# Kernel tuning notes

Measured on AMD Instinct MI355X. Metric: run time of the kernel, lower is better.

The kernel has to match this reference:

```python
import jax, jax.numpy as jnp
import numpy as np

# SamplesLoss('sinkhorn', p=2, blur=0.05, scaling=0.5, diameter=2.0, debias=True, backend='tensorized')
P = 2
BLUR = 0.05
SCALING = 0.5
DIAMETER = 2.0


def epsilon_schedule(p, diameter, blur, scaling):
    # geomloss epsilon annealing: diameter^p -> blur^p, geometric in eps
    eps_list = (
        [diameter ** p]
        + [np.exp(e) for e in np.arange(p * np.log(diameter), p * np.log(blur), p * np.log(scaling))]
        + [blur ** p]
    )
    return [float(e) for e in eps_list]


def softmin(eps, C, h):
    # soft C-transform: f_i = -eps * log sum_j exp(h_j - C_ij/eps)
    # C: (B,N,M), h: (B,M) -> (B,N)
    return -eps * jax.scipy.special.logsumexp(h[:, None, :] - C / eps, axis=2)


def sq_cost(x, y):
    # SqDist(x,y)/2 : (B,N,D),(B,M,D) -> (B,N,M)
    x2 = jnp.sum(x * x, axis=-1)[:, :, None]
    y2 = jnp.sum(y * y, axis=-1)[:, None, :]
    return (x2 + y2 - 2.0 * jnp.einsum('bnd,bmd->bnm', x, y)) * 0.5


def setup_inputs() -> dict:
    key = jax.random.key(0)
    k1, k2 = jax.random.split(key)
    x = jax.random.uniform(k1, (8, 2048, 3), dtype=jnp.float32)
    y = jax.random.uniform(k2, (8, 2048, 3), dtype=jnp.float32)
    return {"x": x, "y": y}


def reference(x, y):
    B, N, _ = x.shape
    M = y.shape[1]
    # uniform weights (SamplesLoss default when only point clouds are given)
    a_log = jnp.full((B, N), -float(np.log(N)), dtype=x.dtype)
    b_log = jnp.full((B, M), -float(np.log(M)), dtype=y.dtype)

    C_xy = sq_cost(x, y)                 # (B,N,M)
    C_yx = jnp.swapaxes(C_xy, 1, 2)      # (B,M,N)
    C_xx = sq_cost(x, x)                 # (B,N,N) debias term
    C_yy = sq_cost(y, y)                 # (B,M,M) debias term

    eps_list = epsilon_schedule(P, DIAMETER, BLUR, SCALING)

    # initialization at the coarsest temperature (balanced OT: damping = 1)
    eps0 = eps_list[0]
    f_aa = softmin(eps0, C_xx, a_log)
    g_bb = softmin(eps0, C_yy, b_log)
    g_ab = softmin(eps0, C_yx, a_log)
    f_ba = softmin(eps0, C_xy, b_log)

    # symmetric Sinkhorn loop with epsilon scaling (no grad tracked in torch here)
    for eps in eps_list:
        ft_ba = softmin(eps, C_xy, b_log + g_ab / eps)
        gt_ab = softmin(eps, C_yx, a_log + f_ba / eps)
        f_ba = 0.5 * (f_ba + ft_ba)
        g_ab = 0.5 * (g_ab + gt_ab)
        ft_aa = softmin(eps, C_xx, a_log + f_aa / eps)
        gt_bb = softmin(eps, C_yy, b_log + g_bb / eps)
        f_aa = 0.5 * (f_aa + ft_aa)
        g_bb = 0.5 * (g_bb + gt_bb)

    # last extrapolation step, with detached dual potentials (torch .detach())
    eps = eps_list[-1]
    sg = jax.lax.stop_gradient
    f_ba, g_ab = (
        softmin(eps, C_xy, b_log + sg(g_ab) / eps),
        softmin(eps, C_yx, a_log + sg(f_ba) / eps),
    )
    f_aa = softmin(eps, C_xx, a_log + sg(f_aa) / eps)
    g_bb = softmin(eps, C_yy, b_log + sg(g_bb) / eps)

    # debiased Sinkhorn divergence, batch mode -> (B,)
    a = jnp.exp(a_log)
    b = jnp.exp(b_log)
    return jnp.sum(a * (f_ba - f_aa), axis=-1) + jnp.sum(b * (g_ab - g_bb), axis=-1)
```

## Files before the change

kernel.cpp:

```cpp
#include <hip/hip_runtime.h>
#include <math.h>

#define BATCH 8
#define NPTS 2048
#define THREADS 256
#define HALF_COLS 1024
#define TILES_H 32
#define ROWS_PER_BLOCK 64
#define LOG_M 7.62559580411076

typedef __attribute__((ext_vector_type(8)))  __bf16 bf16x8;
typedef __attribute__((ext_vector_type(16))) float  f32x16;

union FragU { unsigned short u[8]; uint4 v; };

__device__ __forceinline__ unsigned short f2bf(float f) {
    union { float f; unsigned u; } x; x.f = f;
    unsigned r = x.u + 0x7FFFu + ((x.u >> 16) & 1u);
    return (unsigned short)(r >> 16);
}
__device__ __forceinline__ float bf2f(unsigned short b) {
    union { unsigned u; float f; } x; x.u = ((unsigned)b) << 16;
    return x.f;
}

__global__ __launch_bounds__(THREADS) void softmin_pass(
    const float* __restrict__ x, const float* __restrict__ y,
    const float* __restrict__ potSrc, float* __restrict__ potDst,
    float sigma, float k2, float inv_k2, float rowc0, int avg, int last,
    float* __restrict__ out)
{
    __shared__ uint4 BF[TILES_H][64];
    __shared__ uint4 AF[2][64];
    __shared__ float NM[ROWS_PER_BLOCK];
    __shared__ float SRED[2][2][32];

    const int type  = blockIdx.z;
    const int batch = blockIdx.y;

    const float* rowP;
    const float* colP;
    int hslot, oslot;
    if (type == 0)      { rowP = x; colP = y; hslot = 1; oslot = 0; }
    else if (type == 1) { rowP = y; colP = x; hslot = 0; oslot = 1; }
    else if (type == 2) { rowP = x; colP = x; hslot = 2; oslot = 2; }
    else                { rowP = y; colP = y; hslot = 3; oslot = 3; }

    rowP += batch * NPTS * 3;
    colP += batch * NPTS * 3;
    const float* hP   = potSrc + (hslot * BATCH + batch) * NPTS;
    const float* oldP = potSrc + (oslot * BATCH + batch) * NPTS;
    float*       outP = potDst + (oslot * BATCH + batch) * NPTS;

    if (threadIdx.x < 128) {
        const int g = threadIdx.x >> 6, idx = threadIdx.x & 63;
        const int row = blockIdx.x * ROWS_PER_BLOCK + g * 32 + (idx & 31);
        float x0 = rowP[3 * row + 0], x1 = rowP[3 * row + 1], x2 = rowP[3 * row + 2];
        float p0 = sigma * (x0 - 0.5f), p1 = sigma * (x1 - 0.5f), p2 = sigma * (x2 - 0.5f);
        unsigned short h0 = f2bf(p0); unsigned short l0 = f2bf(p0 - bf2f(h0));
        unsigned short h1 = f2bf(p1); unsigned short l1 = f2bf(p1 - bf2f(h1));
        unsigned short h2 = f2bf(p2); unsigned short l2 = f2bf(p2 - bf2f(h2));
        FragU f;
        if (idx < 32) {
            f.u[0] = h0; f.u[1] = h0; f.u[2] = l0; f.u[3] = l0;
            f.u[4] = h1; f.u[5] = h1; f.u[6] = l1; f.u[7] = l1;
        } else {
            f.u[0] = h2; f.u[1] = h2; f.u[2] = l2; f.u[3] = l2;
            f.u[4] = 0x3F80; f.u[5] = 0x3F80; f.u[6] = 0x3F80; f.u[7] = 0;
        }
        AF[g][idx] = f.v;
    } else if (threadIdx.x < 128 + ROWS_PER_BLOCK) {
        const int r = threadIdx.x - 128;
        const int i = blockIdx.x * ROWS_PER_BLOCK + r;
        float x0 = rowP[3 * i + 0], x1 = rowP[3 * i + 1], x2 = rowP[3 * i + 2];
        float p0 = x0 - 0.5f, p1 = x1 - 0.5f, p2 = x2 - 0.5f;
        float rowconst = 0.5f * (p0 * p0 + p1 * p1 + p2 * p2) + rowc0;
        NM[r] = (oldP[i] - rowconst) * inv_k2;
    }

    const int lane = threadIdx.x & 63;
    const int wave = threadIdx.x >> 6;
    const int g    = wave >> 1;
    const int c    = wave & 1;
    const int khalf = lane >> 5;

    float s[16];
    #pragma unroll
    for (int r = 0; r < 16; ++r) s[r] = 0.0f;
    bf16x8 af;
    f32x16 nmv;

    for (int h = 0; h < 2; ++h) {
        if (h) __syncthreads();

        for (int jj = threadIdx.x; jj < HALF_COLS; jj += THREADS) {
            const int j = h * HALF_COLS + jj;
            float y0 = colP[3 * j + 0], y1 = colP[3 * j + 1], y2 = colP[3 * j + 2];
            float p0 = y0 - 0.5f, p1 = y1 - 0.5f, p2 = y2 - 0.5f;
            unsigned short h0 = f2bf(p0); unsigned short l0 = f2bf(p0 - bf2f(h0));
            unsigned short h1 = f2bf(p1); unsigned short l1 = f2bf(p1 - bf2f(h1));
            unsigned short h2 = f2bf(p2); unsigned short l2 = f2bf(p2 - bf2f(h2));
            float hhe = sigma * (hP[j] - 0.5f * (p0 * p0 + p1 * p1 + p2 * p2));
            unsigned short hA = f2bf(hhe); float r1 = hhe - bf2f(hA);
            unsigned short hB = f2bf(r1);  float r2 = r1 - bf2f(hB);
            unsigned short hC = f2bf(r2);
            FragU f0, f1;
            f0.u[0] = h0; f0.u[1] = l0; f0.u[2] = h0; f0.u[3] = l0;
            f0.u[4] = h1; f0.u[5] = l1; f0.u[6] = h1; f0.u[7] = l1;
            f1.u[0] = h2; f1.u[1] = l2; f1.u[2] = h2; f1.u[3] = l2;
            f1.u[4] = hA; f1.u[5] = hB; f1.u[6] = hC; f1.u[7] = 0;
            BF[jj >> 5][jj & 31]        = f0.v;
            BF[jj >> 5][32 + (jj & 31)] = f1.v;
        }
        __syncthreads();

        if (h == 0) {
            af = *(const bf16x8*)&AF[g][lane];
            #pragma unroll
            for (int r = 0; r < 16; ++r) {
                const int row = (r & 3) + 8 * (r >> 2) + 4 * khalf;
                nmv[r] = NM[g * 32 + row];
            }
        }

        const int tbase = c * (TILES_H / 2);
        #pragma unroll 2
        for (int t = 0; t < TILES_H / 2; ++t) {
            bf16x8 bf = *(const bf16x8*)&BF[tbase + t][lane];
            f32x16 acc = __builtin_amdgcn_mfma_f32_32x32x16_bf16(af, bf, nmv, 0, 0, 0);
            #pragma unroll
            for (int r = 0; r < 16; ++r)
                s[r] += __builtin_amdgcn_exp2f(acc[r]);
        }
    }

    #pragma unroll
    for (int off = 1; off <= 16; off <<= 1)
        #pragma unroll
        for (int r = 0; r < 16; ++r)
            s[r] += __shfl_xor(s[r], off, 64);

    if ((lane & 31) == 0) {
        #pragma unroll
        for (int r = 0; r < 16; ++r) {
            const int row = (r & 3) + 8 * (r >> 2) + 4 * khalf;
            SRED[g][c][row] = s[r];
        }
    }
    __syncthreads();

    if (threadIdx.x < ROWS_PER_BLOCK) {
        const int p = threadIdx.x >> 5, r = threadIdx.x & 31;
        const int i = blockIdx.x * ROWS_PER_BLOCK + p * 32 + r;
        float sum = SRED[p][0][r] + SRED[p][1][r];
        float oldv = oldP[i];
        float res = oldv - k2 * __log2f(sum);
        outP[i] = avg ? 0.5f * (oldv + res) : res;
        if (last) NM[threadIdx.x] = res;
    }

    if (last) {
        __syncthreads();
        if (wave == 0) {
            float v = NM[lane];
            #pragma unroll
            for (int off = 32; off >= 1; off >>= 1)
                v += __shfl_xor(v, off, 64);
            if (lane == 0) {
                float sign = (type >= 2) ? -1.0f : 1.0f;
                atomicAdd(out + batch, sign * v * (1.0f / NPTS));
            }
        }
    }
}

extern "C" void kernel_launch(void* const* d_in, const int* in_sizes, int n_in,
                              void* d_out, int out_size, void* d_ws, size_t ws_size,
                              hipStream_t stream)
{
    const float* x = (const float*)d_in[0];
    const float* y = (const float*)d_in[1];
    float* out = (float*)d_out;

    const size_t potElems = (size_t)4 * BATCH * NPTS;
    float* P0 = (float*)d_ws;
    float* P1 = P0 + potElems;

    hipMemsetAsync(P0, 0, potElems * sizeof(float), stream);
    hipMemsetAsync(out, 0, BATCH * sizeof(float), stream);

    double epsl[16];
    int ne = 0;
    epsl[ne++] = 4.0;
    const double stop = 2.0 * log(0.05);
    const double step = 2.0 * log(0.5);
    for (double e = 2.0 * log(2.0); e > stop; e += step)
        epsl[ne++] = exp(e);
    epsl[ne++] = 0.05 * 0.05;

    float* src = P0;
    float* dst = P1;
    dim3 grid(NPTS / ROWS_PER_BLOCK, BATCH, 4);

    auto launch = [&](double eps, int avg, int last) {
        float sigma  = (float)(M_LOG2E / eps);
        float k2     = (float)(eps * M_LN2);
        float inv_k2 = (float)(1.0 / (eps * M_LN2));
        float rowc0  = (float)(eps * LOG_M);
        softmin_pass<<<grid, THREADS, 0, stream>>>(
            x, y, src, dst, sigma, k2, inv_k2, rowc0, avg, last, out);
        float* t = src; src = dst; dst = t;
    };

    launch(epsl[0], 0, 0);
    for (int k = 0; k < ne; ++k)
        launch(epsl[k], 1, 0);
    launch(epsl[ne - 1], 0, 1);
}
```

Before: 266.6 us.

## Shrink row block to 32 rows and split columns across four waves

Each block now handles 32 rows instead of 64, and all four waves share one A fragment while each takes a quarter of the column tiles. Column data is staged in four 512-column chunks instead of two 1024-column halves, which halves the shared-memory footprint. This doubles the grid size to spread work over more CUs, at the cost of recomputing the column bf16 fragments twice as often overall and adding more barriers per block.

```diff
diff --git a/kernel.cpp b/kernel.cpp
--- a/kernel.cpp
+++ b/kernel.cpp
@@ -4,9 +4,10 @@
 #define BATCH 8
 #define NPTS 2048
 #define THREADS 256
-#define HALF_COLS 1024
-#define TILES_H 32
-#define ROWS_PER_BLOCK 64
+#define STAGE_COLS 512
+#define TILES_S 16
+#define NSTAGES 4
+#define ROWS_PER_BLOCK 32
 #define LOG_M 7.62559580411076
 
 typedef __attribute__((ext_vector_type(8)))  __bf16 bf16x8;
@@ -30,10 +31,10 @@
     float sigma, float k2, float inv_k2, float rowc0, int avg, int last,
     float* __restrict__ out)
 {
-    __shared__ uint4 BF[TILES_H][64];
-    __shared__ uint4 AF[2][64];
+    __shared__ uint4 BF[TILES_S][64];
+    __shared__ uint4 AF[64];
     __shared__ float NM[ROWS_PER_BLOCK];
-    __shared__ float SRED[2][2][32];
+    __shared__ float SRED[4][32];
 
     const int type  = blockIdx.z;
     const int batch = blockIdx.y;
@@ -52,9 +53,9 @@
     const float* oldP = potSrc + (oslot * BATCH + batch) * NPTS;
     float*       outP = potDst + (oslot * BATCH + batch) * NPTS;
 
-    if (threadIdx.x < 128) {
-        const int g = threadIdx.x >> 6, idx = threadIdx.x & 63;
-        const int row = blockIdx.x * ROWS_PER_BLOCK + g * 32 + (idx & 31);
+    if (threadIdx.x < 64) {
+        const int idx = threadIdx.x;
+        const int row = blockIdx.x * ROWS_PER_BLOCK + (idx & 31);
         float x0 = rowP[3 * row + 0], x1 = rowP[3 * row + 1], x2 = rowP[3 * row + 2];
         float p0 = sigma * (x0 - 0.5f), p1 = sigma * (x1 - 0.5f), p2 = sigma * (x2 - 0.5f);
         unsigned short h0 = f2bf(p0); unsigned short l0 = f2bf(p0 - bf2f(h0));
@@ -68,9 +69,9 @@
             f.u[0] = h2; f.u[1] = h2; f.u[2] = l2; f.u[3] = l2;
             f.u[4] = 0x3F80; f.u[5] = 0x3F80; f.u[6] = 0x3F80; f.u[7] = 0;
         }
-        AF[g][idx] = f.v;
-    } else if (threadIdx.x < 128 + ROWS_PER_BLOCK) {
-        const int r = threadIdx.x - 128;
+        AF[idx] = f.v;
+    } else if (threadIdx.x < 64 + ROWS_PER_BLOCK) {
+        const int r = threadIdx.x - 64;
         const int i = blockIdx.x * ROWS_PER_BLOCK + r;
         float x0 = rowP[3 * i + 0], x1 = rowP[3 * i + 1], x2 = rowP[3 * i + 2];
         float p0 = x0 - 0.5f, p1 = x1 - 0.5f, p2 = x2 - 0.5f;
@@ -78,10 +79,8 @@
         NM[r] = (oldP[i] - rowconst) * inv_k2;
     }
 
-    const int lane = threadIdx.x & 63;
-    const int wave = threadIdx.x >> 6;
-    const int g    = wave >> 1;
-    const int c    = wave & 1;
+    const int lane  = threadIdx.x & 63;
+    const int wave  = threadIdx.x >> 6;
     const int khalf = lane >> 5;
 
     float s[16];
@@ -90,11 +89,11 @@
     bf16x8 af;
     f32x16 nmv;
 
-    for (int h = 0; h < 2; ++h) {
-        if (h) __syncthreads();
-
-        for (int jj = threadIdx.x; jj < HALF_COLS; jj += THREADS) {
-            const int j = h * HALF_COLS + jj;
+    for (int st = 0; st < NSTAGES; ++st) {
+        if (st) __syncthreads();
+
+        for (int jj = threadIdx.x; jj < STAGE_COLS; jj += THREADS) {
+            const int j = st * STAGE_COLS + jj;
             float y0 = colP[3 * j + 0], y1 = colP[3 * j + 1], y2 = colP[3 * j + 2];
             float p0 = y0 - 0.5f, p1 = y1 - 0.5f, p2 = y2 - 0.5f;
             unsigned short h0 = f2bf(p0); unsigned short l0 = f2bf(p0 - bf2f(h0));
@@ -114,18 +113,18 @@
         }
         __syncthreads();
 
-        if (h == 0) {
-            af = *(const bf16x8*)&AF[g][lane];
+        if (st == 0) {
+            af = *(const bf16x8*)&AF[lane];
             #pragma unroll
             for (int r = 0; r < 16; ++r) {
                 const int row = (r & 3) + 8 * (r >> 2) + 4 * khalf;
-                nmv[r] = NM[g * 32 + row];
+                nmv[r] = NM[row];
             }
         }
 
-        const int tbase = c * (TILES_H / 2);
-        #pragma unroll 2
-        for (int t = 0; t < TILES_H / 2; ++t) {
+        const int tbase = wave * (TILES_S / 4);
+        #pragma unroll
+        for (int t = 0; t < TILES_S / 4; ++t) {
             bf16x8 bf = *(const bf16x8*)&BF[tbase + t][lane];
             f32x16 acc = __builtin_amdgcn_mfma_f32_32x32x16_bf16(af, bf, nmv, 0, 0, 0);
             #pragma unroll
@@ -144,25 +143,25 @@
         #pragma unroll
         for (int r = 0; r < 16; ++r) {
             const int row = (r & 3) + 8 * (r >> 2) + 4 * khalf;
-            SRED[g][c][row] = s[r];
+            SRED[wave][row] = s[r];
         }
     }
     __syncthreads();
 
     if (threadIdx.x < ROWS_PER_BLOCK) {
-        const int p = threadIdx.x >> 5, r = threadIdx.x & 31;
-        const int i = blockIdx.x * ROWS_PER_BLOCK + p * 32 + r;
-        float sum = SRED[p][0][r] + SRED[p][1][r];
+        const int rr = threadIdx.x;
+        const int i = blockIdx.x * ROWS_PER_BLOCK + rr;
+        float sum = SRED[0][rr] + SRED[1][rr] + SRED[2][rr] + SRED[3][rr];
         float oldv = oldP[i];
         float res = oldv - k2 * __log2f(sum);
         outP[i] = avg ? 0.5f * (oldv + res) : res;
-        if (last) NM[threadIdx.x] = res;
+        if (last) NM[rr] = res;
     }
 
     if (last) {
         __syncthreads();
         if (wave == 0) {
-            float v = NM[lane];
+            float v = (lane < ROWS_PER_BLOCK) ? NM[lane] : 0.0f;
             #pragma unroll
             for (int off = 32; off >= 1; off >>= 1)
                 v += __shfl_xor(v, off, 64);
```

New measurement: 346.6 us. +30.0%, slower.
